# Kernel optimization log

Hardware: AMD Instinct MI355X
Metric: run time of the kernel (lower is better)

Reference implementation:

```python
import jax, jax.numpy as jnp
import numpy as np

D_MODEL = 1024
N_HEADS = 16
D_KEY = 64
ALIBI_SLOPE = 8.0
B, S = 2, 2048


def setup_inputs() -> dict:
    key = jax.random.key(0)
    ks = jax.random.split(key, 10)
    sd = D_MODEL ** -0.5
    states = jax.random.normal(ks[0], (B, S, D_MODEL), dtype=jnp.float32)
    bias_mask = jax.random.normal(ks[1], (B, S, S), dtype=jnp.float32)
    # non-trainable ALiBi-style per-head scale
    head_scale = jnp.exp2(-((jnp.arange(N_HEADS, dtype=jnp.float32) + 1.0) * ALIBI_SLOPE / N_HEADS))
    # parameters (torch Linear: y = x @ W.T + b)
    Wa = jax.random.normal(ks[2], (N_HEADS, D_MODEL), dtype=jnp.float32) * sd  # a_proj, no bias
    Wv = jax.random.normal(ks[3], (D_MODEL, D_MODEL), dtype=jnp.float32) * sd
    bv = jnp.zeros((D_MODEL,), dtype=jnp.float32)
    Wg = jax.random.normal(ks[4], (N_HEADS, D_MODEL), dtype=jnp.float32) * sd
    bg = jnp.zeros((N_HEADS,), dtype=jnp.float32)
    Wo = jax.random.normal(ks[5], (D_MODEL, D_MODEL), dtype=jnp.float32) * sd
    bo = jnp.zeros((D_MODEL,), dtype=jnp.float32)
    return {"states": states, "bias_mask": bias_mask, "head_scale": head_scale,
            "Wa": Wa, "Wv": Wv, "bv": bv, "Wg": Wg, "bg": bg, "Wo": Wo, "bo": bo}


def reference(states, bias_mask, head_scale, Wa, Wv, bv, Wg, bg, Wo, bo):
    # bias: [B,1,Q,K] * [1,H,1,1] -> [B,H,Q,K]
    bias = bias_mask[:, None, :, :] * head_scale[None, :, None, None]
    # values: [B,K,H,dk]
    v = (jnp.einsum('bkm,dm->bkd', states, Wv) + bv).reshape(states.shape[0], states.shape[1], N_HEADS, D_KEY)
    # key-only scores: [B,S,H] -> [B,H,1,K], plus bias -> [B,H,Q,K]
    a = jnp.einsum('bkm,hm->bhk', states, Wa)[:, :, None, :] + bias
    a = jax.nn.softmax(a, axis=-1)
    o = jnp.einsum('bhqk,bkhd->bqhd', a, v)
    g = jnp.einsum('bqm,hm->bqh', states, Wg) + bg
    o = o * jax.nn.sigmoid(g)[..., None]
    o = o.reshape(o.shape[0], o.shape[1], D_MODEL)
    return jnp.einsum('bqm,dm->bqd', o, Wo) + bo
```

## Files before the change

### kernel.cpp

```cpp
#include <hip/hip_runtime.h>


#define LOG2E 1.44269504088896f

using f16   = _Float16;
using f16x4 = __attribute__((ext_vector_type(4))) _Float16;
using f16x8 = __attribute__((ext_vector_type(8))) _Float16;
using f32x4 = __attribute__((ext_vector_type(4))) float;

#define GLDS16(g, l) __builtin_amdgcn_global_load_lds((const __attribute__((address_space(1))) void*)(g), (__attribute__((address_space(3))) void*)(l), 16, 0, 0)

__global__ __launch_bounds__(256) void k_prep(
    const float* __restrict__ states, const float* __restrict__ mask,
    const float* __restrict__ Wa, const float* __restrict__ Wv,
    const float* __restrict__ Wg, const float* __restrict__ Wo,
    f16* __restrict__ st16, f16* __restrict__ Wv16, f16* __restrict__ Wo16,
    f16* __restrict__ Wag16, float* __restrict__ partial)
{
  __shared__ float ws4[4];
  const int bid = blockIdx.x;
  const int t   = threadIdx.x;
  if (bid < 1024) {
    const int row = bid * 4 + (t >> 6);
    const int lane = t & 63;
    const float* sp = states + (size_t)row * 1024 + lane * 16;
    float4 v0 = ((const float4*)sp)[0];
    float4 v1 = ((const float4*)sp)[1];
    float4 v2 = ((const float4*)sp)[2];
    float4 v3 = ((const float4*)sp)[3];
    f16x8 h0, h1;
    h0[0]=(f16)v0.x; h0[1]=(f16)v0.y; h0[2]=(f16)v0.z; h0[3]=(f16)v0.w;
    h0[4]=(f16)v1.x; h0[5]=(f16)v1.y; h0[6]=(f16)v1.z; h0[7]=(f16)v1.w;
    h1[0]=(f16)v2.x; h1[1]=(f16)v2.y; h1[2]=(f16)v2.z; h1[3]=(f16)v2.w;
    h1[4]=(f16)v3.x; h1[5]=(f16)v3.y; h1[6]=(f16)v3.z; h1[7]=(f16)v3.w;
    f16* dp = st16 + (size_t)row * 1024 + lane * 16;
    *(f16x8*)dp = h0; *(f16x8*)(dp + 8) = h1;
  } else {
    const int cb = bid - 1024;
    {
      int idx = cb * 2048 + t * 8;
      const float* src; f16* dst;
      if (idx < 1048576)      { src = Wv + idx;             dst = Wv16 + idx; }
      else if (idx < 2097152) { src = Wo + (idx - 1048576); dst = Wo16 + (idx - 1048576); }
      else { int j = idx - 2097152;
             src = (j < 16384) ? (Wa + j) : (Wg + (j - 16384));
             dst = Wag16 + j; }
      float4 v0 = ((const float4*)src)[0];
      float4 v1 = ((const float4*)src)[1];
      f16x8 h;
      h[0]=(f16)v0.x; h[1]=(f16)v0.y; h[2]=(f16)v0.z; h[3]=(f16)v0.w;
      h[4]=(f16)v1.x; h[5]=(f16)v1.y; h[6]=(f16)v1.z; h[7]=(f16)v1.w;
      *(f16x8*)dst = h;
    }
    if (cb < 512) {
      const float4* mp = (const float4*)(mask + (size_t)cb * 16384);
      float mx = 0.f;
      for (int i = 0; i < 16; ++i) {
        float4 v = mp[t + i * 256];
        mx = fmaxf(mx, fmaxf(fmaxf(fabsf(v.x), fabsf(v.y)), fmaxf(fabsf(v.z), fabsf(v.w))));
      }
      #pragma unroll
      for (int off = 32; off; off >>= 1) mx = fmaxf(mx, __shfl_xor(mx, off, 64));
      if ((t & 63) == 0) ws4[t >> 6] = mx;
      __syncthreads();
      if (t == 0) partial[cb] = fmaxf(fmaxf(ws4[0], ws4[1]), fmaxf(ws4[2], ws4[3]));
    }
  }
}

__global__ __launch_bounds__(256) void k_vg(
    const f16* __restrict__ A, const f16* __restrict__ Bw,
    const float* __restrict__ bv, f16* __restrict__ vt,
    const f16* __restrict__ Bag, const float* __restrict__ bg,
    f16* __restrict__ s16, float* __restrict__ gsig, float* __restrict__ partialS)
{
  __shared__ f16 As[2 * 4096], Bs[2 * 2048];
  const int t = threadIdx.x, wid = t >> 6, lane = t & 63;
  const int lane15 = lane & 15, lg = lane >> 4;
  const int sswz = ((t & 3) ^ ((t >> 3) & 3)) * 8;

  if (blockIdx.x < 32) {
    const int bi = blockIdx.x;
    const int r0 = bi * 128;
    const int b  = bi >> 4;
    const int wm = wid >> 1, wn = wid & 1;
    f32x4 acc[4] = {};
    const f16* ga0 = A  + (size_t)(r0 + (t >> 2)) * 1024      + sswz;
    const f16* ga1 = A  + (size_t)(r0 + 64 + (t >> 2)) * 1024 + sswz;
    const f16* gb0 = Bag + (size_t)(t >> 2) * 1024            + sswz;
    int ra[4], rb;
    #pragma unroll
    for (int m = 0; m < 4; ++m) { int r_ = wm*64 + m*16 + lane15; ra[m] = r_*32 + ((lg ^ ((r_>>1)&3)) * 8); }
    { int r_ = wn*16 + lane15; rb = r_*32 + ((lg ^ ((r_>>1)&3)) * 8); }

    #define STAGE_SG(kt, bb) do { const int k0_ = (kt) * 32; \
        GLDS16(ga0 + k0_, As + (bb)*4096 + wid*512); \
        GLDS16(ga1 + k0_, As + (bb)*4096 + 2048 + wid*512); \
        if (wid < 2) GLDS16(gb0 + k0_, Bs + (bb)*1024 + wid*512); } while(0)
    STAGE_SG(0, 0);
    for (int kt = 0; kt < 32; ++kt) {
      const int cur = kt & 1;
      if (kt < 31) {
        STAGE_SG(kt + 1, cur ^ 1);
        if (wid < 2) asm volatile("s_waitcnt vmcnt(3)" ::: "memory");
        else         asm volatile("s_waitcnt vmcnt(2)" ::: "memory");
      } else {
        asm volatile("s_waitcnt vmcnt(0)" ::: "memory");
      }
      __builtin_amdgcn_s_barrier();
      f16x8 a[4], bf;
      #pragma unroll
      for (int m = 0; m < 4; ++m) a[m] = *(const f16x8*)(As + cur*4096 + ra[m]);
      bf = *(const f16x8*)(Bs + cur*1024 + rb);
      #pragma unroll
      for (int m = 0; m < 4; ++m)
        acc[m] = __builtin_amdgcn_mfma_f32_16x16x32_f16(a[m], bf, acc[m], 0, 0, 0);
      asm volatile("s_waitcnt lgkmcnt(0)" ::: "memory");
      __builtin_amdgcn_s_barrier();
    }
    #undef STAGE_SG
    const int c = wn * 16 + lane15;
    if (wn == 0) {
      float mx = -1e30f;
      #pragma unroll
      for (int m = 0; m < 4; ++m) {
        const int q0 = (r0 & 2047) + wm * 64 + m * 16 + lg * 4;
        f16x4 hv;
        #pragma unroll
        for (int r = 0; r < 4; ++r) { mx = fmaxf(mx, acc[m][r]); hv[r] = (f16)acc[m][r]; }
        *(f16x4*)(s16 + (size_t)(b * 16 + c) * 2048 + q0) = hv;
      }
      mx = fmaxf(mx, __shfl_xor(mx, 16, 64));
      mx = fmaxf(mx, __shfl_xor(mx, 32, 64));
      if (lg == 0) partialS[(bi * 2 + wm) * 16 + c] = mx;
    } else {
      const float bgv = bg[c - 16];
      #pragma unroll
      for (int m = 0; m < 4; ++m) {
        const int q0 = (r0 & 2047) + wm * 64 + m * 16 + lg * 4;
        #pragma unroll
        for (int r = 0; r < 4; ++r) {
          const float g = acc[m][r] + bgv;
          gsig[(size_t)(b * 2048 + q0 + r) * 16 + (c - 16)] = 1.f / (1.f + __expf(-g));
        }
      }
    }
    return;
  }

  const int p = blockIdx.x - 32;
  const int l = (p & 7) * 64 + (p >> 3);
  const int r0 = (l >> 4) * 128, n0 = (l & 15) * 64;
  const int wr = wid >> 1, wc = wid & 1;
  f32x4 acc[4][2] = {};
  const f16* ga0 = A  + (size_t)(r0 + (t >> 2)) * 1024       + sswz;
  const f16* ga1 = A  + (size_t)(r0 + 64 + (t >> 2)) * 1024  + sswz;
  const f16* gb0 = Bw + (size_t)(n0 + (t >> 2)) * 1024       + sswz;
  int ra[4], rb[2];
  #pragma unroll
  for (int m = 0; m < 4; ++m) { int r_ = wr*64 + m*16 + lane15; ra[m] = r_*32 + ((lg ^ ((r_>>1)&3)) * 8); }
  #pragma unroll
  for (int n = 0; n < 2; ++n) { int r_ = wc*32 + n*16 + lane15; rb[n] = r_*32 + ((lg ^ ((r_>>1)&3)) * 8); }

  #define STAGE_G(kt, bb) do { const int k0_ = (kt) * 32; \
      GLDS16(ga0 + k0_, As + (bb)*4096 + wid*512); \
      GLDS16(ga1 + k0_, As + (bb)*4096 + 2048 + wid*512); \
      GLDS16(gb0 + k0_, Bs + (bb)*2048 + wid*512); } while(0)
  STAGE_G(0, 0);
  for (int kt = 0; kt < 32; ++kt) {
    const int cur = kt & 1;
    if (kt < 31) {
      STAGE_G(kt + 1, cur ^ 1);
      asm volatile("s_waitcnt vmcnt(3)" ::: "memory");
    } else {
      asm volatile("s_waitcnt vmcnt(0)" ::: "memory");
    }
    __builtin_amdgcn_s_barrier();
    f16x8 a[4], bf[2];
    #pragma unroll
    for (int m = 0; m < 4; ++m) a[m] = *(const f16x8*)(As + cur*4096 + ra[m]);
    #pragma unroll
    for (int n = 0; n < 2; ++n) bf[n] = *(const f16x8*)(Bs + cur*2048 + rb[n]);
    #pragma unroll
    for (int m = 0; m < 4; ++m)
      #pragma unroll
      for (int n = 0; n < 2; ++n)
        acc[m][n] = __builtin_amdgcn_mfma_f32_16x16x32_f16(a[m], bf[n], acc[m][n], 0, 0, 0);
    asm volatile("s_waitcnt lgkmcnt(0)" ::: "memory");
    __builtin_amdgcn_s_barrier();
  }
  #undef STAGE_G
  const int b_ = r0 >> 11;
  #pragma unroll
  for (int n = 0; n < 2; ++n) {
    const int gn = n0 + wc * 32 + n * 16 + lane15;
    const float bvv = bv[gn];
    #pragma unroll
    for (int m = 0; m < 4; ++m) {
      const int kb = (r0 & 2047) + wr * 64 + m * 16 + lg * 4;
      f16x4 hv;
      #pragma unroll
      for (int r = 0; r < 4; ++r) hv[r] = (f16)(acc[m][n][r] + bvv);
      *(f16x4*)(vt + (size_t)(b_ * 1024 + gn) * 2048 + kb) = hv;
    }
  }
}

__global__ __launch_bounds__(64) void k_lmax(
    const float* __restrict__ partialS, const float* __restrict__ partial,
    const float* __restrict__ hs, float* __restrict__ Lbuf)
{
  const int bh = blockIdx.x, l = threadIdx.x;
  const int b = bh >> 4, h = bh & 15;
  float mx = -1e30f;
  if (l < 32) mx = partialS[((b * 16 + (l >> 1)) * 2 + (l & 1)) * 16 + h];
  float mm = 0.f;
  for (int i = l; i < 256; i += 64) mm = fmaxf(mm, partial[b * 256 + i]);
  #pragma unroll
  for (int off = 32; off; off >>= 1) {
    mx = fmaxf(mx, __shfl_xor(mx, off, 64));
    mm = fmaxf(mm, __shfl_xor(mm, off, 64));
  }
  if (l == 0) Lbuf[bh] = mx + hs[h] * mm;
}

__global__ __launch_bounds__(256, 4) void k_attn(
    const float* __restrict__ mask, const f16* __restrict__ s16,
    const float* __restrict__ gsig, const float* __restrict__ hs,
    const float* __restrict__ Lbuf, const f16* __restrict__ vt,
    f16* __restrict__ og)
{
  __shared__ __align__(16) f16 mks[2 * 4096];
  __shared__ __align__(16) f16 vs[2 * 4096];

  const int p = blockIdx.x;
  const int l = (p & 7) * 128 + (p >> 3);
  const int b = l >> 9, rr = l & 511;
  const int qt = rr >> 4, h = rr & 15;

  const int t = threadIdx.x, wid = t >> 6, lane = t & 63;
  const int lane15 = lane & 15, lg = lane >> 4;
  const float L   = Lbuf[b * 16 + h];
  const float c2  = hs[h] * LOG2E;
  const float nLc = -L * LOG2E;

  const f16* vtb = vt + (size_t)(b * 1024 + h * 64) * 2048;
  const int q16 = wid * 16 + lane15;

  const int mrow = t >> 2;
  const float* msrc = mask + (size_t)b * 4194304 + (size_t)(qt * 64 + mrow) * 2048 + (t & 3) * 16;
  const f16* sptr = s16 + (size_t)(b * 16 + h) * 2048 + lg * 8;

  const int mw0 = mrow * 64 + ((((t & 3) * 2    ) ^ (mrow & 7)) * 8);
  const int mw1 = mrow * 64 + ((((t & 3) * 2 + 1) ^ (mrow & 7)) * 8);
  const int mr0 = q16 * 64 + (((    lg) ^ (q16 & 7)) * 8);
  const int mr1 = q16 * 64 + (((4 + lg) ^ (q16 & 7)) * 8);

  const int vswz = ((t & 7) ^ ((t >> 3) & 7)) * 8;
  const f16* vsrc0 = vtb + (size_t)(     (t >> 3)) * 2048 + vswz;
  const f16* vsrc1 = vtb + (size_t)(32 + (t >> 3)) * 2048 + vswz;
  int voff[2][4];
  #pragma unroll
  for (int kk = 0; kk < 2; ++kk)
    #pragma unroll
    for (int n = 0; n < 4; ++n)
      voff[kk][n] = (n * 16 + lane15) * 64 + (((kk * 4 + lg) ^ (lane15 & 7)) * 8);

  f32x4 acc[4] = {};
  float den = 0.f;
  f32x4 mg0, mg1, mg2, mg3;

  #define MLOAD(KV) do { \
    mg0 = *(const f32x4*)(msrc + (KV));      mg1 = *(const f32x4*)(msrc + (KV) + 4); \
    mg2 = *(const f32x4*)(msrc + (KV) + 8);  mg3 = *(const f32x4*)(msrc + (KV) + 12); } while (0)

  #define MWRITE(BB) do { \
    f16x8 h0_, h1_; \
    h0_[0]=(f16)mg0[0]; h0_[1]=(f16)mg0[1]; h0_[2]=(f16)mg0[2]; h0_[3]=(f16)mg0[3]; \
    h0_[4]=(f16)mg1[0]; h0_[5]=(f16)mg1[1]; h0_[6]=(f16)mg1[2]; h0_[7]=(f16)mg1[3]; \
    h1_[0]=(f16)mg2[0]; h1_[1]=(f16)mg2[1]; h1_[2]=(f16)mg2[2]; h1_[3]=(f16)mg2[3]; \
    h1_[4]=(f16)mg3[0]; h1_[5]=(f16)mg3[1]; h1_[6]=(f16)mg3[2]; h1_[7]=(f16)mg3[3]; \
    *(f16x8*)(mks + (BB)*4096 + mw0) = h0_; \
    *(f16x8*)(mks + (BB)*4096 + mw1) = h1_; } while (0)

  #define STAGE_V(KV, BB) do { \
    GLDS16(vsrc0 + (KV), vs + (BB)*4096 +        wid*512); \
    GLDS16(vsrc1 + (KV), vs + (BB)*4096 + 2048 + wid*512); } while (0)

  #define KKBODY(KK, SH, CUR) do { \
    f16x8 mh = *(const f16x8*)(mks + (CUR)*4096 + ((KK) ? mr1 : mr0)); \
    f16x8 vf0 = *(const f16x8*)(vs + (CUR)*4096 + voff[KK][0]); \
    f16x8 vf1 = *(const f16x8*)(vs + (CUR)*4096 + voff[KK][1]); \
    f16x8 vf2 = *(const f16x8*)(vs + (CUR)*4096 + voff[KK][2]); \
    f16x8 vf3 = *(const f16x8*)(vs + (CUR)*4096 + voff[KK][3]); \
    f16x8 af; float dl_ = 0.f; \
    _Pragma("unroll") \
    for (int j_ = 0; j_ < 8; ++j_) { \
      float sxj = fmaf((float)SH[j_], LOG2E, nLc); \
      float w_ = __builtin_amdgcn_exp2f(fmaf(c2, (float)mh[j_], sxj)); \
      dl_ += w_; af[j_] = (f16)w_; \
    } \
    den += dl_; \
    acc[0] = __builtin_amdgcn_mfma_f32_16x16x32_f16(af, vf0, acc[0], 0, 0, 0); \
    acc[1] = __builtin_amdgcn_mfma_f32_16x16x32_f16(af, vf1, acc[1], 0, 0, 0); \
    acc[2] = __builtin_amdgcn_mfma_f32_16x16x32_f16(af, vf2, acc[2], 0, 0, 0); \
    acc[3] = __builtin_amdgcn_mfma_f32_16x16x32_f16(af, vf3, acc[3], 0, 0, 0); } while (0)

  MLOAD(0);
  STAGE_V(0, 0);
  asm volatile("s_waitcnt vmcnt(2)" ::: "memory");
  MWRITE(0);
  asm volatile("s_waitcnt lgkmcnt(0)" ::: "memory");

  #pragma unroll 1
  for (int kt = 0; kt < 32; ++kt) {
    const int kv = kt * 64;
    const int cur = kt & 1;
    f16x8 s0r = *(const f16x8*)(sptr + kv);
    f16x8 s1r = *(const f16x8*)(sptr + kv + 32);
    if (kt < 31) {
      MLOAD(kv + 64);
      STAGE_V(kv + 64, cur ^ 1);
      asm volatile("s_waitcnt vmcnt(8)" ::: "memory");
    } else {
      asm volatile("s_waitcnt vmcnt(2)" ::: "memory");
    }
    __builtin_amdgcn_s_barrier();
    __builtin_amdgcn_s_setprio(1);
    KKBODY(0, s0r, cur);
    KKBODY(1, s1r, cur);
    __builtin_amdgcn_s_setprio(0);
    if (kt < 31) {
      asm volatile("s_waitcnt vmcnt(2)" ::: "memory");
      MWRITE(cur ^ 1);
    }
    asm volatile("s_waitcnt lgkmcnt(0)" ::: "memory");
    __builtin_amdgcn_s_barrier();
  }
  #undef KKBODY
  #undef STAGE_V
  #undef MWRITE
  #undef MLOAD

  den += __shfl_xor(den, 16, 64);
  den += __shfl_xor(den, 32, 64);

  #pragma unroll
  for (int r = 0; r < 4; ++r) {
    const int ql = lg * 4 + r;
    const int q = qt * 64 + wid * 16 + ql;
    const float dq = __shfl(den, ql, 64);
    const float sc = gsig[(size_t)(b * 2048 + q) * 16 + h] / dq;
    #pragma unroll
    for (int n = 0; n < 4; ++n)
      og[(size_t)(b * 2048 + q) * 1024 + h * 64 + n * 16 + lane15] = (f16)(acc[n][r] * sc);
  }
}

__global__ __launch_bounds__(256) void k_gemm_out(
    const f16* __restrict__ A, const f16* __restrict__ Bw,
    const float* __restrict__ bo, float* __restrict__ out)
{
  __shared__ f16 As[2 * 4096], Bs[2 * 2048];
  const int p = blockIdx.x;
  const int l = (p & 7) * 64 + (p >> 3);
  const int r0 = (l >> 4) * 128, n0 = (l & 15) * 64;
  const int t = threadIdx.x, wid = t >> 6, lane = t & 63;
  const int lane15 = lane & 15, lg = lane >> 4;
  const int wr = wid >> 1, wc = wid & 1;
  f32x4 acc[4][2] = {};
  const int sswz = ((t & 3) ^ ((t >> 3) & 3)) * 8;
  const f16* ga0 = A  + (size_t)(r0 + (t >> 2)) * 1024       + sswz;
  const f16* ga1 = A  + (size_t)(r0 + 64 + (t >> 2)) * 1024  + sswz;
  const f16* gb0 = Bw + (size_t)(n0 + (t >> 2)) * 1024       + sswz;
  int ra[4], rb[2];
  #pragma unroll
  for (int m = 0; m < 4; ++m) { int r_ = wr*64 + m*16 + lane15; ra[m] = r_*32 + ((lg ^ ((r_>>1)&3)) * 8); }
  #pragma unroll
  for (int n = 0; n < 2; ++n) { int r_ = wc*32 + n*16 + lane15; rb[n] = r_*32 + ((lg ^ ((r_>>1)&3)) * 8); }

  #define STAGE_G(kt, bb) do { const int k0_ = (kt) * 32; \
      GLDS16(ga0 + k0_, As + (bb)*4096 + wid*512); \
      GLDS16(ga1 + k0_, As + (bb)*4096 + 2048 + wid*512); \
      GLDS16(gb0 + k0_, Bs + (bb)*2048 + wid*512); } while(0)
  STAGE_G(0, 0);
  for (int kt = 0; kt < 32; ++kt) {
    const int cur = kt & 1;
    if (kt < 31) {
      STAGE_G(kt + 1, cur ^ 1);
      asm volatile("s_waitcnt vmcnt(3)" ::: "memory");
    } else {
      asm volatile("s_waitcnt vmcnt(0)" ::: "memory");
    }
    __builtin_amdgcn_s_barrier();
    f16x8 a[4], bf[2];
    #pragma unroll
    for (int m = 0; m < 4; ++m) a[m] = *(const f16x8*)(As + cur*4096 + ra[m]);
    #pragma unroll
    for (int n = 0; n < 2; ++n) bf[n] = *(const f16x8*)(Bs + cur*2048 + rb[n]);
    #pragma unroll
    for (int m = 0; m < 4; ++m)
      #pragma unroll
      for (int n = 0; n < 2; ++n)
        acc[m][n] = __builtin_amdgcn_mfma_f32_16x16x32_f16(a[m], bf[n], acc[m][n], 0, 0, 0);
    asm volatile("s_waitcnt lgkmcnt(0)" ::: "memory");
    __builtin_amdgcn_s_barrier();
  }
  #undef STAGE_G
  #pragma unroll
  for (int n = 0; n < 2; ++n) {
    const int gn = n0 + wc * 32 + n * 16 + lane15;
    const float bov = bo[gn];
    #pragma unroll
    for (int m = 0; m < 4; ++m) {
      const int rbase = r0 + wr * 64 + m * 16 + lg * 4;
      #pragma unroll
      for (int r = 0; r < 4; ++r)
        out[(size_t)(rbase + r) * 1024 + gn] = acc[m][n][r] + bov;
    }
  }
}

extern "C" void kernel_launch(void* const* d_in, const int* in_sizes, int n_in,
                              void* d_out, int out_size, void* d_ws, size_t ws_size,
                              hipStream_t stream)
{
  const float* states = (const float*)d_in[0];
  const float* mask   = (const float*)d_in[1];
  const float* hs     = (const float*)d_in[2];
  const float* Wa     = (const float*)d_in[3];
  const float* Wv     = (const float*)d_in[4];
  const float* bv     = (const float*)d_in[5];
  const float* Wg     = (const float*)d_in[6];
  const float* bg     = (const float*)d_in[7];
  const float* Wo     = (const float*)d_in[8];
  const float* bo     = (const float*)d_in[9];
  float* out = (float*)d_out;

  char* ws = (char*)d_ws;
  f16*   st16     = (f16*)(ws);
  f16*   og       = (f16*)(ws);
  f16*   Wv16     = (f16*)(ws + 8388608);
  f16*   Wo16     = (f16*)(ws + 10485760);
  f16*   Wag16    = (f16*)(ws + 12582912);
  float* gsig     = (float*)(ws + 12648448);
  f16*   s16      = (f16*)(ws + 12910592);
  float* partial  = (float*)(ws + 13041664);
  float* partialS = (float*)(ws + 13043712);
  float* Lbuf     = (float*)(ws + 13047808);
  f16*   vt       = (f16*)(ws + 13107200);

  k_prep<<<2064, 256, 0, stream>>>(states, mask, Wa, Wv, Wg, Wo,
                                   st16, Wv16, Wo16, Wag16, partial);
  k_vg<<<544, 256, 0, stream>>>(st16, Wv16, bv, vt, Wag16, bg, s16, gsig, partialS);
  k_lmax<<<32, 64, 0, stream>>>(partialS, partial, hs, Lbuf);
  k_attn<<<1024, 256, 0, stream>>>(mask, s16, gsig, hs, Lbuf, vt, og);
  k_gemm_out<<<512, 256, 0, stream>>>(og, Wo16, bo, out);
}
```

Baseline: 121.3 us.

## Precompute shifted fp32 key scores and compute softmax denominator via MFMA

After: 128.6 us. 1.06x slower.

```diff
diff --git a/kernel.cpp b/kernel.cpp
--- a/kernel.cpp
+++ b/kernel.cpp
@@ -6,6 +6,7 @@
 using f16   = _Float16;
 using f16x4 = __attribute__((ext_vector_type(4))) _Float16;
 using f16x8 = __attribute__((ext_vector_type(8))) _Float16;
+using h16x2 = __attribute__((ext_vector_type(2))) __fp16;
 using f32x4 = __attribute__((ext_vector_type(4))) float;
 
 #define GLDS16(g, l) __builtin_amdgcn_global_load_lds((const __attribute__((address_space(1))) void*)(g), (__attribute__((address_space(3))) void*)(l), 16, 0, 0)
@@ -208,7 +209,8 @@
 
 __global__ __launch_bounds__(64) void k_lmax(
     const float* __restrict__ partialS, const float* __restrict__ partial,
-    const float* __restrict__ hs, float* __restrict__ Lbuf)
+    const float* __restrict__ hs, const f16* __restrict__ s16,
+    float* __restrict__ s32L)
 {
   const int bh = blockIdx.x, l = threadIdx.x;
   const int b = bh >> 4, h = bh & 15;
@@ -221,14 +223,17 @@
     mx = fmaxf(mx, __shfl_xor(mx, off, 64));
     mm = fmaxf(mm, __shfl_xor(mm, off, 64));
   }
-  if (l == 0) Lbuf[bh] = mx + hs[h] * mm;
+  const float nL = -(mx + hs[h] * mm) * LOG2E;
+  for (int j = 0; j < 32; ++j) {
+    const int i = j * 64 + l;
+    s32L[(size_t)bh * 2048 + i] = fmaf((float)s16[(size_t)bh * 2048 + i], LOG2E, nL);
+  }
 }
 
 __global__ __launch_bounds__(256, 4) void k_attn(
-    const float* __restrict__ mask, const f16* __restrict__ s16,
+    const float* __restrict__ mask, const float* __restrict__ s32L,
     const float* __restrict__ gsig, const float* __restrict__ hs,
-    const float* __restrict__ Lbuf, const f16* __restrict__ vt,
-    f16* __restrict__ og)
+    const f16* __restrict__ vt, f16* __restrict__ og)
 {
   __shared__ __align__(16) f16 mks[2 * 4096];
   __shared__ __align__(16) f16 vs[2 * 4096];
@@ -240,16 +245,14 @@
 
   const int t = threadIdx.x, wid = t >> 6, lane = t & 63;
   const int lane15 = lane & 15, lg = lane >> 4;
-  const float L   = Lbuf[b * 16 + h];
-  const float c2  = hs[h] * LOG2E;
-  const float nLc = -L * LOG2E;
+  const float c2 = hs[h] * LOG2E;
 
   const f16* vtb = vt + (size_t)(b * 1024 + h * 64) * 2048;
   const int q16 = wid * 16 + lane15;
 
   const int mrow = t >> 2;
   const float* msrc = mask + (size_t)b * 4194304 + (size_t)(qt * 64 + mrow) * 2048 + (t & 3) * 16;
-  const f16* sptr = s16 + (size_t)(b * 16 + h) * 2048 + lg * 8;
+  const float* sptr = s32L + (size_t)(b * 16 + h) * 2048 + lg * 8;
 
   const int mw0 = mrow * 64 + ((((t & 3) * 2    ) ^ (mrow & 7)) * 8);
   const int mw1 = mrow * 64 + ((((t & 3) * 2 + 1) ^ (mrow & 7)) * 8);
@@ -267,12 +270,21 @@
       voff[kk][n] = (n * 16 + lane15) * 64 + (((kk * 4 + lg) ^ (lane15 & 7)) * 8);
 
   f32x4 acc[4] = {};
-  float den = 0.f;
+  f32x4 accd = {};
+  f16x8 vones;
+  #pragma unroll
+  for (int j = 0; j < 8; ++j) vones[j] = (f16)1.0f;
+
   f32x4 mg0, mg1, mg2, mg3;
+  f32x4 sv0, sv1, sv2, sv3;
 
   #define MLOAD(KV) do { \
     mg0 = *(const f32x4*)(msrc + (KV));      mg1 = *(const f32x4*)(msrc + (KV) + 4); \
     mg2 = *(const f32x4*)(msrc + (KV) + 8);  mg3 = *(const f32x4*)(msrc + (KV) + 12); } while (0)
+
+  #define SLOAD(KV) do { \
+    sv0 = *(const f32x4*)(sptr + (KV));      sv1 = *(const f32x4*)(sptr + (KV) + 4); \
+    sv2 = *(const f32x4*)(sptr + (KV) + 32); sv3 = *(const f32x4*)(sptr + (KV) + 36); } while (0)
 
   #define MWRITE(BB) do { \
     f16x8 h0_, h1_; \
@@ -287,24 +299,31 @@
     GLDS16(vsrc0 + (KV), vs + (BB)*4096 +        wid*512); \
     GLDS16(vsrc1 + (KV), vs + (BB)*4096 + 2048 + wid*512); } while (0)
 
-  #define KKBODY(KK, SH, CUR) do { \
+  #define KKBODY(KK, SA, SB, CUR) do { \
     f16x8 mh = *(const f16x8*)(mks + (CUR)*4096 + ((KK) ? mr1 : mr0)); \
     f16x8 vf0 = *(const f16x8*)(vs + (CUR)*4096 + voff[KK][0]); \
     f16x8 vf1 = *(const f16x8*)(vs + (CUR)*4096 + voff[KK][1]); \
     f16x8 vf2 = *(const f16x8*)(vs + (CUR)*4096 + voff[KK][2]); \
     f16x8 vf3 = *(const f16x8*)(vs + (CUR)*4096 + voff[KK][3]); \
-    f16x8 af; float dl_ = 0.f; \
-    _Pragma("unroll") \
-    for (int j_ = 0; j_ < 8; ++j_) { \
-      float sxj = fmaf((float)SH[j_], LOG2E, nLc); \
-      float w_ = __builtin_amdgcn_exp2f(fmaf(c2, (float)mh[j_], sxj)); \
-      dl_ += w_; af[j_] = (f16)w_; \
-    } \
-    den += dl_; \
+    float w0 = __builtin_amdgcn_exp2f(fmaf(c2, (float)mh[0], SA[0])); \
+    float w1 = __builtin_amdgcn_exp2f(fmaf(c2, (float)mh[1], SA[1])); \
+    float w2 = __builtin_amdgcn_exp2f(fmaf(c2, (float)mh[2], SA[2])); \
+    float w3 = __builtin_amdgcn_exp2f(fmaf(c2, (float)mh[3], SA[3])); \
+    float w4 = __builtin_amdgcn_exp2f(fmaf(c2, (float)mh[4], SB[0])); \
+    float w5 = __builtin_amdgcn_exp2f(fmaf(c2, (float)mh[5], SB[1])); \
+    float w6 = __builtin_amdgcn_exp2f(fmaf(c2, (float)mh[6], SB[2])); \
+    float w7 = __builtin_amdgcn_exp2f(fmaf(c2, (float)mh[7], SB[3])); \
+    union { h16x2 q[4]; f16x8 v; } u_; \
+    u_.q[0] = __builtin_amdgcn_cvt_pkrtz(w0, w1); \
+    u_.q[1] = __builtin_amdgcn_cvt_pkrtz(w2, w3); \
+    u_.q[2] = __builtin_amdgcn_cvt_pkrtz(w4, w5); \
+    u_.q[3] = __builtin_amdgcn_cvt_pkrtz(w6, w7); \
+    f16x8 af = u_.v; \
     acc[0] = __builtin_amdgcn_mfma_f32_16x16x32_f16(af, vf0, acc[0], 0, 0, 0); \
     acc[1] = __builtin_amdgcn_mfma_f32_16x16x32_f16(af, vf1, acc[1], 0, 0, 0); \
     acc[2] = __builtin_amdgcn_mfma_f32_16x16x32_f16(af, vf2, acc[2], 0, 0, 0); \
-    acc[3] = __builtin_amdgcn_mfma_f32_16x16x32_f16(af, vf3, acc[3], 0, 0, 0); } while (0)
+    acc[3] = __builtin_amdgcn_mfma_f32_16x16x32_f16(af, vf3, acc[3], 0, 0, 0); \
+    accd   = __builtin_amdgcn_mfma_f32_16x16x32_f16(af, vones, accd, 0, 0, 0); } while (0)
 
   MLOAD(0);
   STAGE_V(0, 0);
@@ -316,19 +335,18 @@
   for (int kt = 0; kt < 32; ++kt) {
     const int kv = kt * 64;
     const int cur = kt & 1;
-    f16x8 s0r = *(const f16x8*)(sptr + kv);
-    f16x8 s1r = *(const f16x8*)(sptr + kv + 32);
+    SLOAD(kv);
     if (kt < 31) {
       MLOAD(kv + 64);
       STAGE_V(kv + 64, cur ^ 1);
-      asm volatile("s_waitcnt vmcnt(8)" ::: "memory");
+      asm volatile("s_waitcnt vmcnt(10)" ::: "memory");
     } else {
-      asm volatile("s_waitcnt vmcnt(2)" ::: "memory");
+      asm volatile("s_waitcnt vmcnt(4)" ::: "memory");
     }
     __builtin_amdgcn_s_barrier();
     __builtin_amdgcn_s_setprio(1);
-    KKBODY(0, s0r, cur);
-    KKBODY(1, s1r, cur);
+    KKBODY(0, sv0, sv1, cur);
+    KKBODY(1, sv2, sv3, cur);
     __builtin_amdgcn_s_setprio(0);
     if (kt < 31) {
       asm volatile("s_waitcnt vmcnt(2)" ::: "memory");
@@ -340,17 +358,14 @@
   #undef KKBODY
   #undef STAGE_V
   #undef MWRITE
+  #undef SLOAD
   #undef MLOAD
-
-  den += __shfl_xor(den, 16, 64);
-  den += __shfl_xor(den, 32, 64);
 
   #pragma unroll
   for (int r = 0; r < 4; ++r) {
     const int ql = lg * 4 + r;
     const int q = qt * 64 + wid * 16 + ql;
-    const float dq = __shfl(den, ql, 64);
-    const float sc = gsig[(size_t)(b * 2048 + q) * 16 + h] / dq;
+    const float sc = gsig[(size_t)(b * 2048 + q) * 16 + h] / accd[r];
     #pragma unroll
     for (int n = 0; n < 4; ++n)
       og[(size_t)(b * 2048 + q) * 1024 + h * 64 + n * 16 + lane15] = (f16)(acc[n][r] * sc);
@@ -447,13 +462,13 @@
   f16*   s16      = (f16*)(ws + 12910592);
   float* partial  = (float*)(ws + 13041664);
   float* partialS = (float*)(ws + 13043712);
-  float* Lbuf     = (float*)(ws + 13047808);
   f16*   vt       = (f16*)(ws + 13107200);
+  float* s32L     = (float*)(ws + 21495808);
 
   k_prep<<<2064, 256, 0, stream>>>(states, mask, Wa, Wv, Wg, Wo,
                                    st16, Wv16, Wo16, Wag16, partial);
   k_vg<<<544, 256, 0, stream>>>(st16, Wv16, bv, vt, Wag16, bg, s16, gsig, partialS);
-  k_lmax<<<32, 64, 0, stream>>>(partialS, partial, hs, Lbuf);
-  k_attn<<<1024, 256, 0, stream>>>(mask, s16, gsig, hs, Lbuf, vt, og);
+  k_lmax<<<32, 64, 0, stream>>>(partialS, partial, hs, s16, s32L);
+  k_attn<<<1024, 256, 0, stream>>>(mask, s32L, gsig, hs, vt, og);
   k_gemm_out<<<512, 256, 0, stream>>>(og, Wo16, bo, out);
 }
```
